# Kernel optimization log

Measured on AMD Instinct MI355X. Metric: run time of the kernel, lower is better.

Reference implementation:

```python
import jax, jax.numpy as jnp
import numpy as np

ALPHA = 1.702
LIMIT = 7.0


def setup_inputs() -> dict:
    key = jax.random.key(0)
    ks = jax.random.split(key, 6)
    T, H, D, E = 8192, 1024, 1024, 8
    hidden_states = jax.random.normal(ks[0], (T, H), dtype=jnp.float32)
    routing_weights = jax.random.uniform(ks[1], (T, E), dtype=jnp.float32)
    # 0.02 scale keeps activations in a sane range (original uses raw randn params)
    gate_up_proj = jax.random.normal(ks[2], (E, H, 2 * D), dtype=jnp.float32) * 0.02
    gate_up_proj_bias = jax.random.normal(ks[3], (E, 2 * D), dtype=jnp.float32) * 0.02
    down_proj = jax.random.normal(ks[4], (E, D, H), dtype=jnp.float32) * 0.02
    down_proj_bias = jax.random.normal(ks[5], (E, H), dtype=jnp.float32) * 0.02
    return {
        "hidden_states": hidden_states,
        "routing_weights": routing_weights,
        "gate_up_proj": gate_up_proj,
        "gate_up_proj_bias": gate_up_proj_bias,
        "down_proj": down_proj,
        "down_proj_bias": down_proj_bias,
    }


def reference(hidden_states, routing_weights, gate_up_proj, gate_up_proj_bias,
              down_proj, down_proj_bias):
    # hidden_states: [T, H]; routing_weights: [T, E] (batch_size == T in the torch code)
    B, H = hidden_states.shape[0], hidden_states.shape[-1]
    hs = hidden_states.reshape(-1, H)  # [T, H]
    # all-experts batched GEMM: [E, T, 2D]
    gate_up = jnp.einsum('th,ehd->etd', hs, gate_up_proj) + gate_up_proj_bias[:, None, :]
    gate = jnp.minimum(gate_up[..., ::2], LIMIT)          # [E, T, D]
    up = jnp.clip(gate_up[..., 1::2], -LIMIT, LIMIT)      # [E, T, D]
    glu = gate * jax.nn.sigmoid(gate * ALPHA)
    # down projection: [E, T, H]
    next_states = jnp.einsum('etd,edh->eth', (up + 1.0) * glu, down_proj) \
        + down_proj_bias[:, None, :]
    # routing-weighted combine over experts: [T, H]
    out = jnp.einsum('eth,te->th', next_states, routing_weights)
    return out.reshape(B, -1, H)  # [T, 1, H], matching final .view(batch_size, -1, hidden)
```

## Files before the change

kernel.cpp:

```cpp
#include <hip/hip_runtime.h>
#include <hip/hip_bf16.h>

#define T_DIM 8192
#define H_DIM 1024
#define D_DIM 1024
#define E_DIM 8
#define TWO_D 2048
#define K2 8192

#define ALPHA_C 1.702f
#define LIMIT_C 7.0f

typedef __attribute__((ext_vector_type(8))) short s8v;
typedef __attribute__((ext_vector_type(4))) float f4v;

__device__ __forceinline__ void g2l16(const void* g, void* l) {
    __builtin_amdgcn_global_load_lds((const __attribute__((address_space(1))) void*)g,
                                     (__attribute__((address_space(3))) void*)l, 16, 0, 0);
}

__device__ __forceinline__ unsigned short f2bf(float f) {
    __hip_bfloat16 h = __float2bfloat16(f);
    return __builtin_bit_cast(unsigned short, h);
}


__global__ void f32_to_bf16_kernel(const float* __restrict__ in,
                                   unsigned short* __restrict__ out, size_t n) {
    size_t i = ((size_t)blockIdx.x * blockDim.x + threadIdx.x) * 4;
    if (i + 3 < n) {
        float4 v = *(const float4*)(in + i);
        ushort4 o;
        o.x = f2bf(v.x); o.y = f2bf(v.y); o.z = f2bf(v.z); o.w = f2bf(v.w);
        *(ushort4*)(out + i) = o;
    }
}

__global__ void transpose_conv_kernel(const float* __restrict__ in,
                                      unsigned short* __restrict__ out,
                                      int cols, size_t ibs, size_t obs, size_t ors,
                                      int remap) {
    __shared__ float t[32][33];
    const int b = blockIdx.z;
    const int c0 = blockIdx.x * 32, r0 = blockIdx.y * 32;
    const int tx = threadIdx.x & 31, ty = threadIdx.x >> 5;
    const float* ip = in + (size_t)b * ibs;
    #pragma unroll
    for (int i = 0; i < 4; ++i)
        t[ty + i * 8][tx] = ip[(size_t)(r0 + ty + i * 8) * cols + c0 + tx];
    __syncthreads();
    unsigned short* op = out + (size_t)b * obs;
    #pragma unroll
    for (int i = 0; i < 4; ++i) {
        int c = c0 + ty + i * 8;
        int nc = remap ? ((c & ~31) + ((c & 1) << 4) + ((c >> 1) & 15)) : c;
        op[(size_t)nc * ors + r0 + tx] = f2bf(t[tx][ty + i * 8]);
    }
}

__global__ void bias_combine_kernel(const float* __restrict__ rw,
                                    const float* __restrict__ b3,
                                    float* __restrict__ out) {
    const int t = blockIdx.x;
    const int h = threadIdx.x * 4;
    float r[E_DIM];
    #pragma unroll
    for (int e = 0; e < E_DIM; ++e) r[e] = rw[(size_t)t * E_DIM + e];
    float4 v = {0.f, 0.f, 0.f, 0.f};
    #pragma unroll
    for (int e = 0; e < E_DIM; ++e) {
        float4 b = *(const float4*)(b3 + (size_t)e * H_DIM + h);
        v.x += r[e] * b.x; v.y += r[e] * b.y; v.z += r[e] * b.z; v.w += r[e] * b.w;
    }
    *(float4*)(out + (size_t)t * H_DIM + h) = v;
}


__global__ __launch_bounds__(256, 2) void gemm1_kernel(
    const short* __restrict__ Ag0,
    const short* __restrict__ Bg0,
    const float* __restrict__ b1,
    const float* __restrict__ rw,
    __hip_bfloat16* __restrict__ act2)
{
    const int e = blockIdx.z;
    const int mBase = blockIdx.x * 128;
    const int nBase = blockIdx.y * 128;
    const int tid = threadIdx.x;
    const int lane = tid & 63;
    const int wave = tid >> 6;
    const int wm = wave >> 1, wn = wave & 1;
    const int cq = lane & 15, quad = lane >> 4;

    __shared__ __align__(16) short As[128 * 64];
    __shared__ __align__(16) short Bs[128 * 64];

    const short* Ag = Ag0 + (size_t)mBase * H_DIM;
    const short* Bg = Bg0 + ((size_t)e * TWO_D + nBase) * H_DIM;

    f4v acc[4][4];
    #pragma unroll
    for (int mt = 0; mt < 4; ++mt)
        #pragma unroll
        for (int nt = 0; nt < 4; ++nt)
            acc[mt][nt] = (f4v){0.f, 0.f, 0.f, 0.f};

    const int srow8 = lane >> 3;
    const int gco = ((lane & 7) ^ srow8) * 8;
    const int cq7 = cq & 7;

    for (int k0 = 0; k0 < H_DIM; k0 += 64) {
        #pragma unroll
        for (int i = 0; i < 4; ++i) {
            const int r = wave * 32 + i * 8 + srow8;
            g2l16(Ag + (size_t)r * H_DIM + k0 + gco, As + (wave * 32 + i * 8) * 64);
            g2l16(Bg + (size_t)r * H_DIM + k0 + gco, Bs + (wave * 32 + i * 8) * 64);
        }
        __syncthreads();
        #pragma unroll
        for (int h = 0; h < 2; ++h) {
            s8v af[4], bf[4];
            const int pc = (((h << 2) + quad) ^ cq7) * 8;
            #pragma unroll
            for (int i = 0; i < 4; ++i) {
                af[i] = *(const s8v*)(As + (wm * 64 + i * 16 + cq) * 64 + pc);
                bf[i] = *(const s8v*)(Bs + (wn * 64 + i * 16 + cq) * 64 + pc);
            }
            #pragma unroll
            for (int mt = 0; mt < 4; ++mt)
                #pragma unroll
                for (int nt = 0; nt < 4; ++nt)
                    acc[mt][nt] = __builtin_amdgcn_mfma_f32_16x16x32_bf16(
                        af[mt], bf[nt], acc[mt][nt], 0, 0, 0);
        }
        __syncthreads();
    }

    float rwv[4][4];
    #pragma unroll
    for (int mt = 0; mt < 4; ++mt)
        #pragma unroll
        for (int r = 0; r < 4; ++r)
            rwv[mt][r] = rw[(size_t)(mBase + wm * 64 + mt * 16 + quad * 4 + r) * E_DIM + e];

    #pragma unroll
    for (int p = 0; p < 2; ++p) {
        const int j = (((nBase + wn * 64 + p * 32) >> 5) << 4) + cq;
        const float gb = b1[(size_t)e * TWO_D + 2 * j];
        const float ub = b1[(size_t)e * TWO_D + 2 * j + 1];
        #pragma unroll
        for (int mt = 0; mt < 4; ++mt) {
            #pragma unroll
            for (int r = 0; r < 4; ++r) {
                float gate = acc[mt][2 * p][r] + gb;
                float up   = acc[mt][2 * p + 1][r] + ub;
                gate = fminf(gate, LIMIT_C);
                up = fminf(fmaxf(up, -LIMIT_C), LIMIT_C);
                float glu = gate / (1.f + __expf(-ALPHA_C * gate));
                float a = (up + 1.f) * glu * rwv[mt][r];
                const int row = mBase + wm * 64 + mt * 16 + quad * 4 + r;
                act2[(size_t)row * K2 + (size_t)e * D_DIM + j] = __float2bfloat16(a);
            }
        }
    }
}


#define KSLICE 2048

__global__ __launch_bounds__(256, 2) void gemm2_kernel(
    const short* __restrict__ Ag0,
    const short* __restrict__ Bg0,
    float* __restrict__ out)
{
    const int id = blockIdx.x;
    const int nBase = (id & 7) * 128;
    const int mBase = ((id >> 3) & 63) * 128;
    const int kBase = (id >> 9) * KSLICE;
    const int tid = threadIdx.x;
    const int lane = tid & 63;
    const int wave = tid >> 6;
    const int wm = wave >> 1, wn = wave & 1;
    const int cq = lane & 15, quad = lane >> 4;

    __shared__ __align__(16) short As[128 * 64];
    __shared__ __align__(16) short Bs[128 * 64];

    const short* Ag = Ag0 + (size_t)mBase * K2;
    const short* Bg = Bg0 + (size_t)nBase * K2;

    f4v acc[4][4];
    #pragma unroll
    for (int mt = 0; mt < 4; ++mt)
        #pragma unroll
        for (int nt = 0; nt < 4; ++nt)
            acc[mt][nt] = (f4v){0.f, 0.f, 0.f, 0.f};

    const int srow8 = lane >> 3;
    const int gco = ((lane & 7) ^ srow8) * 8;
    const int cq7 = cq & 7;

    for (int k0 = kBase; k0 < kBase + KSLICE; k0 += 64) {
        #pragma unroll
        for (int i = 0; i < 4; ++i) {
            const int r = wave * 32 + i * 8 + srow8;
            g2l16(Ag + (size_t)r * K2 + k0 + gco, As + (wave * 32 + i * 8) * 64);
            g2l16(Bg + (size_t)r * K2 + k0 + gco, Bs + (wave * 32 + i * 8) * 64);
        }
        __syncthreads();
        #pragma unroll
        for (int h = 0; h < 2; ++h) {
            s8v af[4], bf[4];
            const int pc = (((h << 2) + quad) ^ cq7) * 8;
            #pragma unroll
            for (int i = 0; i < 4; ++i) {
                af[i] = *(const s8v*)(As + (wm * 64 + i * 16 + cq) * 64 + pc);
                bf[i] = *(const s8v*)(Bs + (wn * 64 + i * 16 + cq) * 64 + pc);
            }
            #pragma unroll
            for (int mt = 0; mt < 4; ++mt)
                #pragma unroll
                for (int nt = 0; nt < 4; ++nt)
                    acc[mt][nt] = __builtin_amdgcn_mfma_f32_16x16x32_bf16(
                        af[mt], bf[nt], acc[mt][nt], 0, 0, 0);
        }
        __syncthreads();
    }

    #pragma unroll
    for (int mt = 0; mt < 4; ++mt) {
        #pragma unroll
        for (int r = 0; r < 4; ++r) {
            const int row = mBase + wm * 64 + mt * 16 + quad * 4 + r;
            #pragma unroll
            for (int nt = 0; nt < 4; ++nt) {
                atomicAdd(out + (size_t)row * H_DIM + nBase + wn * 64 + nt * 16 + cq,
                          acc[mt][nt][r]);
            }
        }
    }
}


extern "C" void kernel_launch(void* const* d_in, const int* in_sizes, int n_in,
                              void* d_out, int out_size, void* d_ws, size_t ws_size,
                              hipStream_t stream) {
    const float* hs = (const float*)d_in[0];
    const float* rw = (const float*)d_in[1];
    const float* w1 = (const float*)d_in[2];
    const float* b1 = (const float*)d_in[3];
    const float* w3 = (const float*)d_in[4];
    const float* b3 = (const float*)d_in[5];
    float* out = (float*)d_out;

    char* ws = (char*)d_ws;
    unsigned short* hsb  = (unsigned short*)(ws);
    unsigned short* w1b  = (unsigned short*)(ws + ((size_t)16 << 20));
    unsigned short* w3b  = (unsigned short*)(ws + ((size_t)48 << 20));
    unsigned short* act2 = (unsigned short*)(ws + ((size_t)64 << 20));

    {
        size_t n = (size_t)T_DIM * H_DIM;
        f32_to_bf16_kernel<<<dim3(n / (256 * 4)), dim3(256), 0, stream>>>(hs, hsb, n);
    }
    transpose_conv_kernel<<<dim3(TWO_D / 32, H_DIM / 32, E_DIM), dim3(256), 0, stream>>>(
        w1, w1b, TWO_D, (size_t)H_DIM * TWO_D, (size_t)TWO_D * H_DIM, (size_t)H_DIM, 1);
    transpose_conv_kernel<<<dim3(H_DIM / 32, D_DIM / 32, E_DIM), dim3(256), 0, stream>>>(
        w3, w3b, H_DIM, (size_t)D_DIM * H_DIM, (size_t)D_DIM, (size_t)K2, 0);
    gemm1_kernel<<<dim3(T_DIM / 128, TWO_D / 128, E_DIM), dim3(256), 0, stream>>>(
        (const short*)hsb, (const short*)w1b, b1, rw, (__hip_bfloat16*)act2);
    bias_combine_kernel<<<dim3(T_DIM), dim3(H_DIM / 4), 0, stream>>>(rw, b3, out);
    gemm2_kernel<<<dim3(8 * 64 * (K2 / KSLICE)), dim3(256), 0, stream>>>(
        (const short*)act2, (const short*)w3b, out);
}
```

Baseline: 646.9 us.

## Replace split-K atomic adds with bf16 partial buffers and a reduce pass

The down-projection GEMM no longer accumulates its four K-slices into the output with float atomicAdd. Slice 0 now stores its result directly to the output, and slices 1-3 write bf16 partials into workspace regions that are free by then (old hs/w1 staging). A new reduce kernel sums the output and the three partials, then adds the routing-weighted bias, replacing the old bias-init kernel. This removes contended global atomics and their ordering with the bias init, at the cost of an extra read pass and bf16 rounding of three partial sums.

```diff
diff --git a/kernel.cpp b/kernel.cpp
--- a/kernel.cpp
+++ b/kernel.cpp
@@ -22,6 +22,11 @@
 __device__ __forceinline__ unsigned short f2bf(float f) {
     __hip_bfloat16 h = __float2bfloat16(f);
     return __builtin_bit_cast(unsigned short, h);
+}
+
+__device__ __forceinline__ float bf2f(unsigned short u) {
+    unsigned int x = ((unsigned int)u) << 16;
+    return __builtin_bit_cast(float, x);
 }
 
 
@@ -58,21 +63,32 @@
     }
 }
 
-__global__ void bias_combine_kernel(const float* __restrict__ rw,
-                                    const float* __restrict__ b3,
-                                    float* __restrict__ out) {
+__global__ void reduce_bias_kernel(const unsigned short* __restrict__ p0,
+                                   const unsigned short* __restrict__ p1,
+                                   const unsigned short* __restrict__ p2,
+                                   const float* __restrict__ rw,
+                                   const float* __restrict__ b3,
+                                   float* __restrict__ out) {
     const int t = blockIdx.x;
     const int h = threadIdx.x * 4;
+    const size_t idx = (size_t)t * H_DIM + h;
     float r[E_DIM];
     #pragma unroll
     for (int e = 0; e < E_DIM; ++e) r[e] = rw[(size_t)t * E_DIM + e];
-    float4 v = {0.f, 0.f, 0.f, 0.f};
+    float4 v = *(const float4*)(out + idx);
+    ushort4 a = *(const ushort4*)(p0 + idx);
+    ushort4 b = *(const ushort4*)(p1 + idx);
+    ushort4 c = *(const ushort4*)(p2 + idx);
+    v.x += bf2f(a.x) + bf2f(b.x) + bf2f(c.x);
+    v.y += bf2f(a.y) + bf2f(b.y) + bf2f(c.y);
+    v.z += bf2f(a.z) + bf2f(b.z) + bf2f(c.z);
+    v.w += bf2f(a.w) + bf2f(b.w) + bf2f(c.w);
     #pragma unroll
     for (int e = 0; e < E_DIM; ++e) {
-        float4 b = *(const float4*)(b3 + (size_t)e * H_DIM + h);
-        v.x += r[e] * b.x; v.y += r[e] * b.y; v.z += r[e] * b.z; v.w += r[e] * b.w;
-    }
-    *(float4*)(out + (size_t)t * H_DIM + h) = v;
+        float4 bb = *(const float4*)(b3 + (size_t)e * H_DIM + h);
+        v.x += r[e] * bb.x; v.y += r[e] * bb.y; v.z += r[e] * bb.z; v.w += r[e] * bb.w;
+    }
+    *(float4*)(out + idx) = v;
 }
 
 
@@ -171,12 +187,16 @@
 __global__ __launch_bounds__(256, 2) void gemm2_kernel(
     const short* __restrict__ Ag0,
     const short* __restrict__ Bg0,
-    float* __restrict__ out)
+    float* __restrict__ out,
+    unsigned short* __restrict__ p0,
+    unsigned short* __restrict__ p1,
+    unsigned short* __restrict__ p2)
 {
     const int id = blockIdx.x;
     const int nBase = (id & 7) * 128;
     const int mBase = ((id >> 3) & 63) * 128;
-    const int kBase = (id >> 9) * KSLICE;
+    const int kIdx = id >> 9;
+    const int kBase = kIdx * KSLICE;
     const int tid = threadIdx.x;
     const int lane = tid & 63;
     const int wave = tid >> 6;
@@ -227,16 +247,20 @@
         __syncthreads();
     }
 
+    unsigned short* pdst = (kIdx == 1) ? p0 : (kIdx == 2) ? p1 : p2;
     #pragma unroll
     for (int mt = 0; mt < 4; ++mt) {
         #pragma unroll
         for (int r = 0; r < 4; ++r) {
             const int row = mBase + wm * 64 + mt * 16 + quad * 4 + r;
+            const size_t idx = (size_t)row * H_DIM + nBase + wn * 64 + 16 * 0 + cq;
             #pragma unroll
             for (int nt = 0; nt < 4; ++nt) {
-                atomicAdd(out + (size_t)row * H_DIM + nBase + wn * 64 + nt * 16 + cq,
-                          acc[mt][nt][r]);
+                const size_t o = (size_t)row * H_DIM + nBase + wn * 64 + nt * 16 + cq;
+                if (kIdx == 0) out[o] = acc[mt][nt][r];
+                else           pdst[o] = f2bf(acc[mt][nt][r]);
             }
+            (void)idx;
         }
     }
 }
@@ -258,6 +282,9 @@
     unsigned short* w1b  = (unsigned short*)(ws + ((size_t)16 << 20));
     unsigned short* w3b  = (unsigned short*)(ws + ((size_t)48 << 20));
     unsigned short* act2 = (unsigned short*)(ws + ((size_t)64 << 20));
+    unsigned short* p0 = (unsigned short*)(ws);
+    unsigned short* p1 = (unsigned short*)(ws + ((size_t)16 << 20));
+    unsigned short* p2 = (unsigned short*)(ws + ((size_t)32 << 20));
 
     {
         size_t n = (size_t)T_DIM * H_DIM;
@@ -269,7 +296,8 @@
         w3, w3b, H_DIM, (size_t)D_DIM * H_DIM, (size_t)D_DIM, (size_t)K2, 0);
     gemm1_kernel<<<dim3(T_DIM / 128, TWO_D / 128, E_DIM), dim3(256), 0, stream>>>(
         (const short*)hsb, (const short*)w1b, b1, rw, (__hip_bfloat16*)act2);
-    bias_combine_kernel<<<dim3(T_DIM), dim3(H_DIM / 4), 0, stream>>>(rw, b3, out);
-    gemm2_kernel<<<dim3(8 * 64 * (K2 / KSLICE)), dim3(256), 0, stream>>>(
-        (const short*)act2, (const short*)w3b, out);
-}
+    gemm2_kernel<<<dim3(8 * 64 * 4), dim3(256), 0, stream>>>(
+        (const short*)act2, (const short*)w3b, out, p0, p1, p2);
+    reduce_bias_kernel<<<dim3(T_DIM), dim3(H_DIM / 4), 0, stream>>>(
+        p0, p1, p2, rw, b3, out);
+}
```

New measurement: 623.4 us. -3.6%, faster.
